# Kernel tuning notes

Measured on AMD Instinct MI355X. Metric: run time of the kernel, lower is better.

## Reference

```python
import jax, jax.numpy as jnp
import numpy as np

NUM_SAMPLES = 2048
MAX_AGENTS = 64
D_MODEL = 128
NUM_HEADS = 8


def setup_inputs() -> dict:
    key = jax.random.key(0)
    # deterministic ragged sizes: 1..64 repeating -> total = 32 * (64*65/2) = 66560
    agents = ((np.arange(NUM_SAMPLES) % MAX_AGENTS) + 1).astype(np.int32)
    total = int(agents.sum())
    k1, k2, k3 = jax.random.split(key, 3)
    s = 1.0 / np.sqrt(D_MODEL)
    return {
        "att_in": jax.random.normal(k1, (total, D_MODEL), jnp.float32),
        "in_proj_w": jax.random.uniform(k2, (3 * D_MODEL, D_MODEL), jnp.float32, -s, s),
        "in_proj_b": jnp.zeros((3 * D_MODEL,), jnp.float32),
        "out_proj_w": jax.random.uniform(k3, (D_MODEL, D_MODEL), jnp.float32, -s, s),
        "out_proj_b": jnp.zeros((D_MODEL,), jnp.float32),
        "agents_per_sample": jnp.asarray(agents),
    }


def reference(att_in, in_proj_w, in_proj_b, out_proj_w, out_proj_b, agents_per_sample):
    # agents_per_sample is static ragged metadata (host ints)
    agents = np.asarray(agents_per_sample)
    B = len(agents)
    A = int(agents.max())
    D = att_in.shape[-1]
    hd = D // NUM_HEADS

    # scatter ragged tokens into zero-padded [B, A, D]
    sample_ids = np.repeat(np.arange(B), agents)
    pos = np.concatenate([np.arange(n) for n in agents])
    padded = jnp.zeros((B, A, D), att_in.dtype).at[sample_ids, pos].set(att_in)
    key_valid = jnp.asarray(np.arange(A)[None, :] < agents[:, None])  # [B, A]

    # torch nn.MultiheadAttention math (eval mode, dropout=0)
    qkv = padded @ in_proj_w.T + in_proj_b  # [B, A, 3D]
    q, k, v = jnp.split(qkv, 3, axis=-1)
    q = q.reshape(B, A, NUM_HEADS, hd)
    k = k.reshape(B, A, NUM_HEADS, hd)
    v = v.reshape(B, A, NUM_HEADS, hd)

    scores = jnp.einsum("bqhd,bkhd->bhqk", q, k) / jnp.sqrt(jnp.asarray(hd, q.dtype))
    scores = jnp.where(key_valid[:, None, None, :], scores, jnp.asarray(-1e30, scores.dtype))
    attn = jax.nn.softmax(scores, axis=-1)

    out = jnp.einsum("bhqk,bkhd->bqhd", attn, v).reshape(B, A, D)
    out = out @ out_proj_w.T + out_proj_b

    # unpad: concatenation of the per-sample ragged outputs
    return out[sample_ids, pos]
```

## Files before the change

kernel.cpp:

```cpp
#include <hip/hip_runtime.h>

#define DM 128
#define NHEADS 8

typedef __attribute__((ext_vector_type(8))) __bf16 bf16x8;
typedef __attribute__((ext_vector_type(8))) unsigned short u16x8;
typedef __attribute__((ext_vector_type(4))) float f32x4;

__device__ inline unsigned short f2bf(float f) {
    unsigned u = __float_as_uint(f);
    u += 0x7FFFu + ((u >> 16) & 1u);
    return (unsigned short)(u >> 16);
}

__global__ void prep(const int* __restrict__ agents, int B,
                     const float* __restrict__ wqkv, const float* __restrict__ wout,
                     int* __restrict__ offs,
                     unsigned short* __restrict__ wqkv_bf,
                     unsigned short* __restrict__ wout_bf) {
    if (blockIdx.x < 64) {
        int idx = (blockIdx.x * 256 + threadIdx.x) * 4;
        if (idx < 49152) {
            float4 v = *(const float4*)(wqkv + idx);
            ushort4 o;
            o.x = f2bf(v.x); o.y = f2bf(v.y); o.z = f2bf(v.z); o.w = f2bf(v.w);
            *(ushort4*)(wqkv_bf + idx) = o;
        } else {
            int j = idx - 49152;
            float4 v = *(const float4*)(wout + j);
            ushort4 o;
            o.x = f2bf(v.x); o.y = f2bf(v.y); o.z = f2bf(v.z); o.w = f2bf(v.w);
            *(ushort4*)(wout_bf + j) = o;
        }
    } else {
        __shared__ int part[256];
        const int tid = threadIdx.x;
        const int per = (B + 255) >> 8;
        const int base = tid * per;
        int s = 0;
        for (int i = 0; i < per; ++i) {
            int idx = base + i;
            if (idx < B) s += agents[idx];
        }
        part[tid] = s;
        __syncthreads();
        for (int off = 1; off < 256; off <<= 1) {
            int v = (tid >= off) ? part[tid - off] : 0;
            __syncthreads();
            part[tid] += v;
            __syncthreads();
        }
        int run = (tid == 0) ? 0 : part[tid - 1];
        for (int i = 0; i < per; ++i) {
            int idx = base + i;
            if (idx < B) { offs[idx] = run; run += agents[idx]; }
        }
    }
}

__launch_bounds__(256, 4)
__global__ void qkv_gemm(const float* __restrict__ x,
                         const unsigned short* __restrict__ wqkvb,
                         const float* __restrict__ bqkv,
                         unsigned short* __restrict__ qws,
                         unsigned short* __restrict__ kv,
                         int M) {
    __shared__ __align__(16) unsigned short Bs[128 * 136];
    __shared__ __align__(16) float biass[128];
    const int bid = blockIdx.x;
    const int seg = bid % 3;
    const int m0 = (bid / 3) * 128;
    const int tid = threadIdx.x;

    for (int f = tid; f < 2048; f += 256) {
        int t = f >> 4, c = f & 15;
        *(uint4*)&Bs[t * 136 + c * 8] =
            *(const uint4*)(wqkvb + (size_t)(seg * 128 + t) * 128 + c * 8);
    }
    if (tid < 32)
        ((float4*)biass)[tid] = ((const float4*)(bqkv + seg * 128))[tid];
    __syncthreads();

    const int wave = tid >> 6, lane = tid & 63, quad = lane >> 4, l16 = lane & 15;
    const int mw = m0 + wave * 32;

    bf16x8 af[2][4];
    #pragma unroll
    for (int mt = 0; mt < 2; ++mt) {
        int row = mw + mt * 16 + l16;
        row = (row < M) ? row : (M - 1);
        const float* xr = x + (size_t)row * DM;
        #pragma unroll
        for (int ks = 0; ks < 4; ++ks) {
            float4 u = *(const float4*)(xr + ks * 32 + quad * 8);
            float4 v = *(const float4*)(xr + ks * 32 + quad * 8 + 4);
            u16x8 t;
            t[0] = f2bf(u.x); t[1] = f2bf(u.y); t[2] = f2bf(u.z); t[3] = f2bf(u.w);
            t[4] = f2bf(v.x); t[5] = f2bf(v.y); t[6] = f2bf(v.z); t[7] = f2bf(v.w);
            af[mt][ks] = __builtin_bit_cast(bf16x8, t);
        }
    }

    unsigned short* obase; int ostride, ocol;
    if (seg == 0) { obase = qws; ostride = 128; ocol = 0; }
    else          { obase = kv;  ostride = 256; ocol = (seg == 2) ? 128 : 0; }

    const int row0 = mw + l16, row1 = row0 + 16;

    for (int ct = 0; ct < 8; ++ct) {
        bf16x8 bc[4];
        #pragma unroll
        for (int ks = 0; ks < 4; ++ks)
            bc[ks] = *(const bf16x8*)&Bs[(ct * 16 + l16) * 136 + ks * 32 + quad * 8];
        f32x4 a0 = {0.f, 0.f, 0.f, 0.f}, a1 = {0.f, 0.f, 0.f, 0.f};
        #pragma unroll
        for (int ks = 0; ks < 4; ++ks) {
            a0 = __builtin_amdgcn_mfma_f32_16x16x32_bf16(bc[ks], af[0][ks], a0, 0, 0, 0);
            a1 = __builtin_amdgcn_mfma_f32_16x16x32_bf16(bc[ks], af[1][ks], a1, 0, 0, 0);
        }
        const int n0 = ct * 16 + quad * 4;
        const float4 b4 = *(const float4*)(biass + n0);
        ushort4 v0, v1;
        v0.x = f2bf(a0[0] + b4.x); v0.y = f2bf(a0[1] + b4.y);
        v0.z = f2bf(a0[2] + b4.z); v0.w = f2bf(a0[3] + b4.w);
        v1.x = f2bf(a1[0] + b4.x); v1.y = f2bf(a1[1] + b4.y);
        v1.z = f2bf(a1[2] + b4.z); v1.w = f2bf(a1[3] + b4.w);
        if (row0 < M) *(ushort4*)(obase + (size_t)row0 * ostride + ocol + n0) = v0;
        if (row1 < M) *(ushort4*)(obase + (size_t)row1 * ostride + ocol + n0) = v1;
    }
}

#define KS_OFF 0
#define VS_OFF 17408
#define PS_OFF 34816
#define SMEM2 53248

__launch_bounds__(512, 6)
__global__ void attn(unsigned short* __restrict__ qa,
                     const unsigned short* __restrict__ kv,
                     const int* __restrict__ agents,
                     const int* __restrict__ offs,
                     int M) {
    __shared__ __align__(16) char smem[SMEM2];
    unsigned short* Ks = (unsigned short*)(smem + KS_OFF);
    unsigned short* Vs = (unsigned short*)(smem + VS_OFF);
    unsigned short* Ps = (unsigned short*)(smem + PS_OFF);

    const int s = blockIdx.x;
    const int n = agents[s];
    const int base = offs[s];
    const int tid = threadIdx.x;
    const int wave = tid >> 6, lane = tid & 63, quad = lane >> 4, l16 = lane & 15;
    const int h = wave;
    const int nkt = (n + 15) >> 4;
    const int nks = (n + 31) >> 5;

    for (int f = tid; f < 3328; f += 512)
        ((uint4*)smem)[f] = make_uint4(0u, 0u, 0u, 0u);
    __syncthreads();

    for (int f = tid; f < n * 16; f += 512) {
        int t = f >> 4, c = f & 15;
        *(uint4*)&Ks[t * 136 + c * 8] = *(const uint4*)(kv + (size_t)(base + t) * 256 + c * 8);
        *(uint4*)&Vs[t * 136 + c * 8] = *(const uint4*)(kv + (size_t)(base + t) * 256 + 128 + c * 8);
    }
    __syncthreads();

    unsigned short* Pw = Ps + wave * 16 * 72;
    const __bf16* Vsb = (const __bf16*)Vs;
    for (int mt = 0; mt < nkt; ++mt) {
        bf16x8 qf = (bf16x8)(__bf16)0.0f;
        if (quad < 2) {
            int qrow = base + mt * 16 + l16;
            qrow = (qrow < M) ? qrow : (M - 1);
            qf = *(const bf16x8*)(qa + (size_t)qrow * 128 + h * 16 + quad * 8);
        }
        f32x4 sc[4];
        #pragma unroll
        for (int kt = 0; kt < 4; ++kt)
            sc[kt] = (f32x4){0.f, 0.f, 0.f, 0.f};
        #pragma unroll
        for (int kt = 0; kt < 4; ++kt) {
            if (kt < nkt) {
                bf16x8 bb = *(const bf16x8*)&Ks[(kt * 16 + l16) * 136 + h * 16 + quad * 8];
                sc[kt] = __builtin_amdgcn_mfma_f32_16x16x32_bf16(qf, bb,
                          (f32x4){0.f, 0.f, 0.f, 0.f}, 0, 0, 0);
            }
        }
        #pragma unroll
        for (int r = 0; r < 4; ++r) {
            float pr[4];
            float mm = -1e30f;
            #pragma unroll
            for (int kt = 0; kt < 4; ++kt) {
                float v = -1e30f;
                if (kt < nkt) {
                    int key = kt * 16 + l16;
                    v = (key < n) ? sc[kt][r] * 0.25f : -1e30f;
                }
                pr[kt] = v;
                mm = fmaxf(mm, v);
            }
            mm = fmaxf(mm, __shfl_xor(mm, 1));
            mm = fmaxf(mm, __shfl_xor(mm, 2));
            mm = fmaxf(mm, __shfl_xor(mm, 4));
            mm = fmaxf(mm, __shfl_xor(mm, 8));
            float ll = 0.f;
            #pragma unroll
            for (int kt = 0; kt < 4; ++kt) {
                if (kt < nkt) {
                    float e = __expf(pr[kt] - mm);
                    pr[kt] = e;
                    ll += e;
                }
            }
            ll += __shfl_xor(ll, 1);
            ll += __shfl_xor(ll, 2);
            ll += __shfl_xor(ll, 4);
            ll += __shfl_xor(ll, 8);
            float inv = 1.0f / ll;
            #pragma unroll
            for (int kt = 0; kt < 4; ++kt)
                if (kt < nkt)
                    Pw[(quad * 4 + r) * 72 + kt * 16 + l16] = f2bf(pr[kt] * inv);
        }
        f32x4 o = {0.f, 0.f, 0.f, 0.f};
        #pragma unroll
        for (int ks2 = 0; ks2 < 2; ++ks2) {
            if (ks2 < nks) {
                bf16x8 a = *(const bf16x8*)&Pw[l16 * 72 + ks2 * 32 + quad * 8];
                bf16x8 bb;
                #pragma unroll
                for (int j = 0; j < 8; ++j)
                    bb[j] = Vsb[(ks2 * 32 + quad * 8 + j) * 136 + h * 16 + l16];
                o = __builtin_amdgcn_mfma_f32_16x16x32_bf16(a, bb, o, 0, 0, 0);
            }
        }
        #pragma unroll
        for (int r = 0; r < 4; ++r) {
            int row = mt * 16 + quad * 4 + r;
            if (row < n)
                qa[(size_t)(base + row) * 128 + h * 16 + l16] = f2bf(o[r]);
        }
    }
}

__launch_bounds__(256, 4)
__global__ void oproj(const unsigned short* __restrict__ attn_b,
                      const unsigned short* __restrict__ woutb,
                      const float* __restrict__ bout,
                      float* __restrict__ out, int M) {
    __shared__ __align__(16) unsigned short Ws[128 * 136];
    __shared__ __align__(16) float biass[128];
    const int m0 = blockIdx.x * 64;
    const int tid = threadIdx.x;

    for (int f = tid; f < 2048; f += 256) {
        int t = f >> 4, c = f & 15;
        *(uint4*)&Ws[t * 136 + c * 8] = *(const uint4*)(woutb + (size_t)t * 128 + c * 8);
    }
    if (tid < 32)
        ((float4*)biass)[tid] = ((const float4*)bout)[tid];
    __syncthreads();

    const int wave = tid >> 6, lane = tid & 63, quad = lane >> 4, l16 = lane & 15;
    const int mw = m0 + wave * 16;

    bf16x8 af[4];
    {
        int row = mw + l16;
        row = (row < M) ? row : (M - 1);
        #pragma unroll
        for (int ks = 0; ks < 4; ++ks)
            af[ks] = *(const bf16x8*)(attn_b + (size_t)row * DM + ks * 32 + quad * 8);
    }

    const int row0 = mw + l16;

    for (int ct = 0; ct < 8; ++ct) {
        bf16x8 bc[4];
        #pragma unroll
        for (int ks = 0; ks < 4; ++ks)
            bc[ks] = *(const bf16x8*)&Ws[(ct * 16 + l16) * 136 + ks * 32 + quad * 8];
        f32x4 a0 = {0.f, 0.f, 0.f, 0.f};
        #pragma unroll
        for (int ks = 0; ks < 4; ++ks)
            a0 = __builtin_amdgcn_mfma_f32_16x16x32_bf16(bc[ks], af[ks], a0, 0, 0, 0);
        const int n0 = ct * 16 + quad * 4;
        const float4 b4 = *(const float4*)(biass + n0);
        float4 o0;
        o0.x = a0[0] + b4.x; o0.y = a0[1] + b4.y; o0.z = a0[2] + b4.z; o0.w = a0[3] + b4.w;
        if (row0 < M) *(float4*)(out + (size_t)row0 * DM + n0) = o0;
    }
}

extern "C" void kernel_launch(void* const* d_in, const int* in_sizes, int n_in,
                              void* d_out, int out_size, void* d_ws, size_t ws_size,
                              hipStream_t stream) {
    const float* att_in     = (const float*)d_in[0];
    const float* in_proj_w  = (const float*)d_in[1];
    const float* in_proj_b  = (const float*)d_in[2];
    const float* out_proj_w = (const float*)d_in[3];
    const float* out_proj_b = (const float*)d_in[4];
    const int*   agents     = (const int*)d_in[5];
    const int B = in_sizes[5];
    const int M = out_size / DM;

    int* offs = (int*)d_ws;
    unsigned short* wqkv_bf = (unsigned short*)((char*)d_ws + 8192);
    unsigned short* wout_bf = (unsigned short*)((char*)d_ws + 106496);
    unsigned short* qbuf    = (unsigned short*)((char*)d_ws + 139264);
    unsigned short* kvbuf   = (unsigned short*)d_out;

    const int strips = (M + 127) / 128;

    hipLaunchKernelGGL(prep, dim3(65), dim3(256), 0, stream,
                       agents, B, in_proj_w, out_proj_w, offs, wqkv_bf, wout_bf);
    hipLaunchKernelGGL(qkv_gemm, dim3(strips * 3), dim3(256), 0, stream,
                       att_in, wqkv_bf, in_proj_b, qbuf, kvbuf, M);
    hipLaunchKernelGGL(attn, dim3(B), dim3(512), 0, stream,
                       qbuf, kvbuf, agents, offs, M);
    hipLaunchKernelGGL(oproj, dim3((M + 63) / 64), dim3(256), 0, stream,
                       qbuf, wout_bf, out_proj_b, (float*)d_out, M);
}
```

Measured before the change: 176.8 us.

## Keep attention K/V and probabilities in registers, drop LDS staging

The attention kernel no longer stages K, V and P through shared memory. Each wave loads its head's K and V fragments straight from global memory into registers and computes scores transposed (K·Q), so softmax reduces across quads with two shuffles instead of four. Probabilities are packed directly into MFMA operands, removing the LDS zeroing, the barriers and the per-row P round trip. It also templates on key count (2 or 4 key tiles), uses exp2 with a prescaled constant and a hardware reciprocal, and prefetches the next Q tile. In exchange it uses more registers and does strided per-element global loads for V.

```diff
diff --git a/kernel.cpp b/kernel.cpp
--- a/kernel.cpp
+++ b/kernel.cpp
@@ -130,10 +130,98 @@
     }
 }
 
-#define KS_OFF 0
-#define VS_OFF 17408
-#define PS_OFF 34816
-#define SMEM2 53248
+template<int K4>
+__device__ __forceinline__ void attn_body(
+    unsigned short* __restrict__ qa,
+    const unsigned short* __restrict__ kv,
+    int n, int base, int M, int h, int quad, int l16)
+{
+    bf16x8 kf[K4];
+    #pragma unroll
+    for (int kt = 0; kt < K4; ++kt) {
+        kf[kt] = (bf16x8)(__bf16)0.0f;
+        if (quad < 2) {
+            int kr = base + kt * 16 + l16;
+            kr = kr < M ? kr : M - 1;
+            kf[kt] = *(const bf16x8*)(kv + (size_t)kr * 256 + h * 16 + quad * 8);
+        }
+    }
+    bf16x8 vA[K4 / 2];
+    #pragma unroll
+    for (int g = 0; g < K4 / 2; ++g)
+        #pragma unroll
+        for (int j = 0; j < 8; ++j) {
+            int vr = base + g * 32 + ((j >> 2) * 16) + quad * 4 + (j & 3);
+            vr = vr < M ? vr : M - 1;
+            vA[g][j] = ((const __bf16*)kv)[(size_t)vr * 256 + 128 + h * 16 + l16];
+        }
+    int thr[K4];
+    #pragma unroll
+    for (int kt = 0; kt < K4; ++kt) {
+        int t = n - kt * 16 - quad * 4;
+        thr[kt] = t < 0 ? 0 : (t > 4 ? 4 : t);
+    }
+    const float SC2 = 0.25f * 1.44269504088896340736f;
+    const int nqt = (n + 15) >> 4;
+
+    int qr0 = base + l16; qr0 = qr0 < M ? qr0 : M - 1;
+    bf16x8 qf = (bf16x8)(__bf16)0.0f;
+    if (quad < 2) qf = *(const bf16x8*)(qa + (size_t)qr0 * 128 + h * 16 + quad * 8);
+
+    for (int mt = 0; mt < nqt; ++mt) {
+        bf16x8 qn = (bf16x8)(__bf16)0.0f;
+        if (mt + 1 < nqt && quad < 2) {
+            int qr = base + (mt + 1) * 16 + l16;
+            qr = qr < M ? qr : M - 1;
+            qn = *(const bf16x8*)(qa + (size_t)qr * 128 + h * 16 + quad * 8);
+        }
+        float pr[K4][4];
+        float mm = -3.0e38f;
+        #pragma unroll
+        for (int kt = 0; kt < K4; ++kt) {
+            f32x4 sc = __builtin_amdgcn_mfma_f32_16x16x32_bf16(
+                kf[kt], qf, (f32x4){0.f, 0.f, 0.f, 0.f}, 0, 0, 0);
+            #pragma unroll
+            for (int r = 0; r < 4; ++r) {
+                float v = sc[r] * SC2;
+                pr[kt][r] = v;
+                mm = fmaxf(mm, v);
+            }
+        }
+        mm = fmaxf(mm, __shfl_xor(mm, 16));
+        mm = fmaxf(mm, __shfl_xor(mm, 32));
+        float ll = 0.f;
+        #pragma unroll
+        for (int kt = 0; kt < K4; ++kt)
+            #pragma unroll
+            for (int r = 0; r < 4; ++r) {
+                float e = exp2f(pr[kt][r] - mm);
+                e = (r < thr[kt]) ? e : 0.f;
+                pr[kt][r] = e;
+                ll += e;
+            }
+        ll += __shfl_xor(ll, 16);
+        ll += __shfl_xor(ll, 32);
+        float inv = __builtin_amdgcn_rcpf(ll);
+        bf16x8 pf[K4 / 2];
+        #pragma unroll
+        for (int g = 0; g < K4 / 2; ++g)
+            #pragma unroll
+            for (int j = 0; j < 8; ++j)
+                pf[g][j] = (__bf16)(pr[2 * g + (j >> 2)][j & 3] * inv);
+        f32x4 o = __builtin_amdgcn_mfma_f32_16x16x32_bf16(
+            vA[0], pf[0], (f32x4){0.f, 0.f, 0.f, 0.f}, 0, 0, 0);
+        if (K4 == 4)
+            o = __builtin_amdgcn_mfma_f32_16x16x32_bf16(vA[1], pf[1], o, 0, 0, 0);
+        const int row = mt * 16 + l16;
+        if (row < n) {
+            ushort4 w;
+            w.x = f2bf(o[0]); w.y = f2bf(o[1]); w.z = f2bf(o[2]); w.w = f2bf(o[3]);
+            *(ushort4*)(qa + (size_t)(base + row) * 128 + h * 16 + quad * 4) = w;
+        }
+        qf = qn;
+    }
+}
 
 __launch_bounds__(512, 6)
 __global__ void attn(unsigned short* __restrict__ qa,
@@ -141,108 +229,14 @@
                      const int* __restrict__ agents,
                      const int* __restrict__ offs,
                      int M) {
-    __shared__ __align__(16) char smem[SMEM2];
-    unsigned short* Ks = (unsigned short*)(smem + KS_OFF);
-    unsigned short* Vs = (unsigned short*)(smem + VS_OFF);
-    unsigned short* Ps = (unsigned short*)(smem + PS_OFF);
-
     const int s = blockIdx.x;
     const int n = agents[s];
     const int base = offs[s];
     const int tid = threadIdx.x;
-    const int wave = tid >> 6, lane = tid & 63, quad = lane >> 4, l16 = lane & 15;
-    const int h = wave;
-    const int nkt = (n + 15) >> 4;
-    const int nks = (n + 31) >> 5;
-
-    for (int f = tid; f < 3328; f += 512)
-        ((uint4*)smem)[f] = make_uint4(0u, 0u, 0u, 0u);
-    __syncthreads();
-
-    for (int f = tid; f < n * 16; f += 512) {
-        int t = f >> 4, c = f & 15;
-        *(uint4*)&Ks[t * 136 + c * 8] = *(const uint4*)(kv + (size_t)(base + t) * 256 + c * 8);
-        *(uint4*)&Vs[t * 136 + c * 8] = *(const uint4*)(kv + (size_t)(base + t) * 256 + 128 + c * 8);
-    }
-    __syncthreads();
-
-    unsigned short* Pw = Ps + wave * 16 * 72;
-    const __bf16* Vsb = (const __bf16*)Vs;
-    for (int mt = 0; mt < nkt; ++mt) {
-        bf16x8 qf = (bf16x8)(__bf16)0.0f;
-        if (quad < 2) {
-            int qrow = base + mt * 16 + l16;
-            qrow = (qrow < M) ? qrow : (M - 1);
-            qf = *(const bf16x8*)(qa + (size_t)qrow * 128 + h * 16 + quad * 8);
-        }
-        f32x4 sc[4];
-        #pragma unroll
-        for (int kt = 0; kt < 4; ++kt)
-            sc[kt] = (f32x4){0.f, 0.f, 0.f, 0.f};
-        #pragma unroll
-        for (int kt = 0; kt < 4; ++kt) {
-            if (kt < nkt) {
-                bf16x8 bb = *(const bf16x8*)&Ks[(kt * 16 + l16) * 136 + h * 16 + quad * 8];
-                sc[kt] = __builtin_amdgcn_mfma_f32_16x16x32_bf16(qf, bb,
-                          (f32x4){0.f, 0.f, 0.f, 0.f}, 0, 0, 0);
-            }
-        }
-        #pragma unroll
-        for (int r = 0; r < 4; ++r) {
-            float pr[4];
-            float mm = -1e30f;
-            #pragma unroll
-            for (int kt = 0; kt < 4; ++kt) {
-                float v = -1e30f;
-                if (kt < nkt) {
-                    int key = kt * 16 + l16;
-                    v = (key < n) ? sc[kt][r] * 0.25f : -1e30f;
-                }
-                pr[kt] = v;
-                mm = fmaxf(mm, v);
-            }
-            mm = fmaxf(mm, __shfl_xor(mm, 1));
-            mm = fmaxf(mm, __shfl_xor(mm, 2));
-            mm = fmaxf(mm, __shfl_xor(mm, 4));
-            mm = fmaxf(mm, __shfl_xor(mm, 8));
-            float ll = 0.f;
-            #pragma unroll
-            for (int kt = 0; kt < 4; ++kt) {
-                if (kt < nkt) {
-                    float e = __expf(pr[kt] - mm);
-                    pr[kt] = e;
-                    ll += e;
-                }
-            }
-            ll += __shfl_xor(ll, 1);
-            ll += __shfl_xor(ll, 2);
-            ll += __shfl_xor(ll, 4);
-            ll += __shfl_xor(ll, 8);
-            float inv = 1.0f / ll;
-            #pragma unroll
-            for (int kt = 0; kt < 4; ++kt)
-                if (kt < nkt)
-                    Pw[(quad * 4 + r) * 72 + kt * 16 + l16] = f2bf(pr[kt] * inv);
-        }
-        f32x4 o = {0.f, 0.f, 0.f, 0.f};
-        #pragma unroll
-        for (int ks2 = 0; ks2 < 2; ++ks2) {
-            if (ks2 < nks) {
-                bf16x8 a = *(const bf16x8*)&Pw[l16 * 72 + ks2 * 32 + quad * 8];
-                bf16x8 bb;
-                #pragma unroll
-                for (int j = 0; j < 8; ++j)
-                    bb[j] = Vsb[(ks2 * 32 + quad * 8 + j) * 136 + h * 16 + l16];
-                o = __builtin_amdgcn_mfma_f32_16x16x32_bf16(a, bb, o, 0, 0, 0);
-            }
-        }
-        #pragma unroll
-        for (int r = 0; r < 4; ++r) {
-            int row = mt * 16 + quad * 4 + r;
-            if (row < n)
-                qa[(size_t)(base + row) * 128 + h * 16 + l16] = f2bf(o[r]);
-        }
-    }
+    const int h = tid >> 6, lane = tid & 63, quad = (lane >> 4), l16 = lane & 15;
+    (void)lane;
+    if (n > 32) attn_body<4>(qa, kv, n, base, M, h, quad, l16);
+    else        attn_body<2>(qa, kv, n, base, M, h, quad, l16);
 }
 
 __launch_bounds__(256, 4)
```

Measured after the change: 159.0 us. -10.1%, faster.
